# Performance work log

Hardware: AMD Instinct MI355X
Metric: run time of the kernel (lower is better)

Reference implementation:

```python
import jax, jax.numpy as jnp
import numpy as np

H = 64          # heightmap size (sqrt of in_channels=4096)
FEATS = [8, 16, 32, 64]
NEG_SLOPE = 0.01
EPS = 1e-12


def setup_inputs() -> dict:
    key = jax.random.key(0)
    ks = jax.random.split(key, 32)
    inp = {"x": jax.random.normal(ks[0], (16384, H * H), dtype=jnp.float32)}
    in_feat = H
    ki = 1
    for li, out_feat in enumerate(FEATS):
        bound = np.sqrt(6.0 / (in_feat + out_feat))  # xavier_uniform
        inp[f"w{li}"] = jax.random.uniform(ks[ki], (out_feat, in_feat), minval=-bound, maxval=bound, dtype=jnp.float32); ki += 1
        inp[f"b{li}"] = jnp.zeros((out_feat,), dtype=jnp.float32)
        inp[f"s{li}"] = jnp.ones((1,), dtype=jnp.float32)  # sigma parameter
        in_feat = out_feat
    compress_in = H * FEATS[-1]
    inp["wm0"] = jax.random.normal(ks[ki], (80, compress_in), dtype=jnp.float32) * 0.02; ki += 1
    inp["bm0"] = jnp.zeros((80,), dtype=jnp.float32)
    inp["wm1"] = jax.random.normal(ks[ki], (60, 80), dtype=jnp.float32) * 0.02; ki += 1
    inp["bm1"] = jnp.zeros((60,), dtype=jnp.float32)
    return inp


def _gauss_layer(x, dist_sq, sigma, w, b):
    # x: [B, H, Cin] ; dist_sq: [H, H] ; w: [Cout, Cin]
    xp = jnp.einsum('bhc,oc->bho', x, w) + b
    k = jnp.exp(-dist_sq / (2.0 * sigma[0] ** 2))                 # [H, H]
    k = k / jnp.maximum(jnp.sum(k, axis=-1, keepdims=True), EPS)  # L1 normalize
    out = jnp.einsum('ij,bjc->bic', k, xp)
    return jax.nn.leaky_relu(out, NEG_SLOPE)


def reference(x, w0, b0, s0, w1, b1, s1, w2, b2, s2, w3, b3, s3, wm0, bm0, wm1, bm1):
    B = x.shape[0]
    h = x.reshape(B, H, H)
    idx = jnp.arange(H, dtype=x.dtype)
    dist_sq = (idx[:, None] - idx[None, :]) ** 2  # coords are 1-D row indices
    for sigma, w, b in ((s0, w0, b0), (s1, w1, b1), (s2, w2, b2), (s3, w3, b3)):
        h = _gauss_layer(h, dist_sq, sigma, w, b)
    h = h.reshape(B, -1)                              # [B, H*64]
    h = jax.nn.leaky_relu(h @ wm0.T + bm0, NEG_SLOPE)
    h = jax.nn.leaky_relu(h @ wm1.T + bm1, NEG_SLOPE)
    return h
```

## Files before the change

kernel.cpp:

```cpp
#include <hip/hip_runtime.h>


typedef _Float16 f16x8 __attribute__((ext_vector_type(8)));
typedef _Float16 f16x4 __attribute__((ext_vector_type(4)));
typedef __fp16   hf2   __attribute__((ext_vector_type(2)));
typedef float    f32x4 __attribute__((ext_vector_type(4)));

#define KT_OFF    327680
#define W0P_OFF   344064
#define W1P_OFF   345088
#define W2P_OFF   345344
#define W3P_OFF   345856

__global__ void prep_all(const float* __restrict__ s0, const float* __restrict__ s1,
                         const float* __restrict__ s2, const float* __restrict__ s3,
                         const float* __restrict__ w0, const float* __restrict__ w1,
                         const float* __restrict__ w2, const float* __restrict__ w3,
                         const float* __restrict__ wm0, _Float16* __restrict__ base) {
  int bid = blockIdx.x, tid = threadIdx.x;
  if (bid < 1280) {
    int idx = bid * 256 + tid;
    int kc = idx / 2560, rem = idx % 2560;
    int n = rem >> 5, o = rem & 31;
    base[idx] = (_Float16)wm0[n * 4096 + kc * 32 + o];
  } else if (bid == 1280) {
    int li = tid >> 6, i = tid & 63;
    float sg = (li == 0) ? s0[0] : (li == 1) ? s1[0] : (li == 2) ? s2[0] : s3[0];
    float denom = 2.0f * sg * sg;
    float sum = 0.0f;
    for (int j = 0; j < 64; ++j) {
      float d = (float)(i - j);
      sum += expf(-(d * d) / denom);
    }
    float inv = 1.0f / fmaxf(sum, 1e-12f);
    for (int j = 0; j < 64; ++j) {
      float d = (float)(i - j);
      base[KT_OFF + (li * 64 + i) * 64 + j] = (_Float16)(expf(-(d * d) / denom) * inv);
    }
  } else {
    for (int r = tid; r < 3840; r += 256) {
      float v;
      if (r < 1024)      { int o = r >> 6, c = r & 63;             v = (o < 8) ? w0[o * 64 + c] : 0.0f; }
      else if (r < 1280) { int q = r - 1024; int o = q >> 4, c = q & 15; v = (c < 8) ? w1[o * 8 + c] : 0.0f; }
      else if (r < 1792) { int q = r - 1280; int o = q >> 4, c = q & 15; v = w2[o * 16 + c]; }
      else               { int q = r - 1792; int o = q >> 5, c = q & 31; v = w3[o * 32 + c]; }
      base[W0P_OFF + r] = (_Float16)v;
    }
  }
}

__device__ __forceinline__ float leaky(float v) { return v > 0.0f ? v : 0.01f * v; }

__device__ __forceinline__ f16x4 pk4(float a, float b, float c, float d) {
  union { f16x4 v; hf2 p[2]; } u;
  u.p[0] = __builtin_amdgcn_cvt_pkrtz(a, b);
  u.p[1] = __builtin_amdgcn_cvt_pkrtz(c, d);
  return u.v;
}

__device__ __forceinline__ int swz(int sx, int row, int c) {
  return row * 64 + ((((c >> 3) ^ (row & 7) ^ sx) & 7) << 3) + (c & 7);
}

#define DS_FENCE() __builtin_amdgcn_sched_barrier(0x7F)

__device__ __forceinline__ f16x8 ldf(const _Float16* p) { return *(const f16x8*)p; }
__device__ __forceinline__ f16x4 ldf4(const _Float16* p) { return *(const f16x4*)p; }

template<int NT, int KC>
__device__ __forceinline__ void stage_a_pre(_Float16* P, int sx,
                                            const f16x8* wf, const float* bv,
                                            int lo, int hi) {
  DS_FENCE();
  f16x8 a[4][KC];
#pragma unroll
  for (int mt = 0; mt < 4; ++mt)
#pragma unroll
    for (int kc = 0; kc < KC; ++kc)
      a[mt][kc] = ldf(P + swz(sx, mt * 16 + lo, kc * 32 + hi * 8));
  DS_FENCE();
#pragma unroll
  for (int mt = 0; mt < 4; ++mt)
#pragma unroll
    for (int nt = 0; nt < NT; ++nt) {
      f32x4 acc = {bv[nt], bv[nt], bv[nt], bv[nt]};
#pragma unroll
      for (int kc = 0; kc < KC; ++kc)
        acc = __builtin_amdgcn_mfma_f32_16x16x32_f16(a[mt][kc], wf[nt * KC + kc], acc, 0, 0, 0);
      *(f16x4*)(P + swz(sx, nt * 16 + lo, mt * 16 + hi * 4)) =
          pk4(acc[0], acc[1], acc[2], acc[3]);
    }
}

template<int NT>
__device__ __forceinline__ void stage_a16_pre(_Float16* P, int sx,
                                              const f16x4* wf, const float* bv,
                                              int lo, int hi) {
  DS_FENCE();
  f16x4 a[4];
#pragma unroll
  for (int mt = 0; mt < 4; ++mt)
    a[mt] = ldf4(P + swz(sx, mt * 16 + lo, hi * 4));
  DS_FENCE();
#pragma unroll
  for (int mt = 0; mt < 4; ++mt)
#pragma unroll
    for (int nt = 0; nt < NT; ++nt) {
      f32x4 acc = {bv[nt], bv[nt], bv[nt], bv[nt]};
      acc = __builtin_amdgcn_mfma_f32_16x16x16f16(a[mt], wf[nt], acc, 0, 0, 0);
      *(f16x4*)(P + swz(sx, nt * 16 + lo, mt * 16 + hi * 4)) =
          pk4(acc[0], acc[1], acc[2], acc[3]);
    }
}

template<int MT>
__device__ __forceinline__ void stage_b_pre(_Float16* P, int sx,
                                            const f16x8* kb, int lo, int hi) {
  DS_FENCE();
  f16x8 ax[MT][2];
#pragma unroll
  for (int ot = 0; ot < MT; ++ot)
#pragma unroll
    for (int kc = 0; kc < 2; ++kc)
      ax[ot][kc] = ldf(P + swz(sx, ot * 16 + lo, kc * 32 + hi * 8));
  DS_FENCE();
#pragma unroll
  for (int ot = 0; ot < MT; ++ot)
#pragma unroll
    for (int nt = 0; nt < 4; ++nt) {
      f32x4 acc = {0.0f, 0.0f, 0.0f, 0.0f};
#pragma unroll
      for (int kc = 0; kc < 2; ++kc)
        acc = __builtin_amdgcn_mfma_f32_16x16x32_f16(ax[ot][kc], kb[nt * 2 + kc], acc, 0, 0, 0);
      *(f16x4*)(P + swz(sx, nt * 16 + lo, ot * 16 + hi * 4)) =
          pk4(leaky(acc[0]), leaky(acc[1]), leaky(acc[2]), leaky(acc[3]));
    }
}

__global__ __launch_bounds__(1024, 4)
void fused(const float* __restrict__ x,
           const float* __restrict__ bb0, const float* __restrict__ bb1,
           const float* __restrict__ bb2, const float* __restrict__ bb3,
           const _Float16* __restrict__ wsh,
           const float* __restrict__ bm0, const float* __restrict__ wm1,
           const float* __restrict__ bm1, float* __restrict__ out, int B) {
  __shared__ _Float16 lds[16][4096];
  const int tid = threadIdx.x;
  const int wv = tid >> 6, lane = tid & 63;
  const int lo = lane & 15, hi = lane >> 4;
  const int smp0 = blockIdx.x * 16;
  int smp = smp0 + wv;  if (smp >= B) smp = B - 1;
  _Float16* P = lds[wv];
  const int sx = wv;
  const _Float16* kt = wsh + KT_OFF;

  float bv0 = (lo < 8) ? bb0[lo] : 0.0f;
  float bv1 = bb1[lo];
  float bv2[2] = {bb2[lo], bb2[16 + lo]};
  float bv3[4] = {bb3[lo], bb3[16 + lo], bb3[32 + lo], bb3[48 + lo]};

  f16x8 wf0[2];
#pragma unroll
  for (int kc = 0; kc < 2; ++kc)
    wf0[kc] = ldf(wsh + W0P_OFF + lo * 64 + kc * 32 + hi * 8);
  f16x8 kbA[8];
#pragma unroll
  for (int nt = 0; nt < 4; ++nt)
#pragma unroll
    for (int kc = 0; kc < 2; ++kc)
      kbA[nt * 2 + kc] = ldf(kt + 0 * 4096 + (nt * 16 + lo) * 64 + kc * 32 + hi * 8);

  const float* xr = x + (size_t)smp * 4096;
  f16x8 a0[4][2];
#pragma unroll
  for (int mt = 0; mt < 4; ++mt)
#pragma unroll
    for (int kc = 0; kc < 2; ++kc) {
      const float4* p4 = (const float4*)(xr + (mt * 16 + lo) * 64 + kc * 32 + hi * 8);
      float4 v0 = p4[0], v1 = p4[1];
      union { f16x8 v; hf2 p[4]; } u;
      u.p[0] = __builtin_amdgcn_cvt_pkrtz(v0.x, v0.y);
      u.p[1] = __builtin_amdgcn_cvt_pkrtz(v0.z, v0.w);
      u.p[2] = __builtin_amdgcn_cvt_pkrtz(v1.x, v1.y);
      u.p[3] = __builtin_amdgcn_cvt_pkrtz(v1.z, v1.w);
      a0[mt][kc] = u.v;
    }
  DS_FENCE();
#pragma unroll
  for (int mt = 0; mt < 4; ++mt) {
    f32x4 acc = {bv0, bv0, bv0, bv0};
#pragma unroll
    for (int kc = 0; kc < 2; ++kc)
      acc = __builtin_amdgcn_mfma_f32_16x16x32_f16(a0[mt][kc], wf0[kc], acc, 0, 0, 0);
    *(f16x4*)(P + swz(sx, lo, mt * 16 + hi * 4)) =
        pk4(acc[0], acc[1], acc[2], acc[3]);
  }

  f16x4 wfA1[1];
  wfA1[0] = ldf4(wsh + W1P_OFF + lo * 16 + hi * 4);
  stage_b_pre<1>(P, sx, kbA, lo, hi);

  f16x8 kbB[8];
#pragma unroll
  for (int nt = 0; nt < 4; ++nt)
#pragma unroll
    for (int kc = 0; kc < 2; ++kc)
      kbB[nt * 2 + kc] = ldf(kt + 1 * 4096 + (nt * 16 + lo) * 64 + kc * 32 + hi * 8);
  stage_a16_pre<1>(P, sx, wfA1, &bv1, lo, hi);

  f16x4 wfA2[2];
#pragma unroll
  for (int nt = 0; nt < 2; ++nt)
    wfA2[nt] = ldf4(wsh + W2P_OFF + (nt * 16 + lo) * 16 + hi * 4);
  stage_b_pre<1>(P, sx, kbB, lo, hi);

  f16x8 kbC[8];
#pragma unroll
  for (int nt = 0; nt < 4; ++nt)
#pragma unroll
    for (int kc = 0; kc < 2; ++kc)
      kbC[nt * 2 + kc] = ldf(kt + 2 * 4096 + (nt * 16 + lo) * 64 + kc * 32 + hi * 8);
  stage_a16_pre<2>(P, sx, wfA2, bv2, lo, hi);

  f16x8 wfA3[4];
#pragma unroll
  for (int nt = 0; nt < 4; ++nt)
    wfA3[nt] = ldf(wsh + W3P_OFF + (nt * 16 + lo) * 32 + hi * 8);
  stage_b_pre<2>(P, sx, kbC, lo, hi);

  f16x8 kbD[8];
#pragma unroll
  for (int nt = 0; nt < 4; ++nt)
#pragma unroll
    for (int kc = 0; kc < 2; ++kc)
      kbD[nt * 2 + kc] = ldf(kt + 3 * 4096 + (nt * 16 + lo) * 64 + kc * 32 + hi * 8);
  stage_a_pre<4, 1>(P, sx, wfA3, bv3, lo, hi);

  stage_b_pre<4>(P, sx, kbD, lo, hi);

  __syncthreads();

  f32x4 acc[5];
#pragma unroll
  for (int nt = 0; nt < 5; ++nt) { f32x4 z = {0.0f, 0.0f, 0.0f, 0.0f}; acc[nt] = z; }

  const _Float16* ap = &lds[lo][0];
#pragma unroll 2
  for (int it = 0; it < 8; ++it) {
    int kc = wv * 8 + it;
    int row = kc >> 1, cc = (kc & 1) * 32 + hi * 8;
    f16x8 a = *(const f16x8*)(ap + swz(lo, row, cc));
    const _Float16* bp = wsh + (size_t)kc * 2560 + lo * 32 + hi * 8;
#pragma unroll
    for (int nt = 0; nt < 5; ++nt) {
      f16x8 b = *(const f16x8*)(bp + nt * 512);
      acc[nt] = __builtin_amdgcn_mfma_f32_16x16x32_f16(a, b, acc[nt], 0, 0, 0);
    }
  }
  __syncthreads();

  float* scr = (float*)&lds[0][0];
#pragma unroll
  for (int nt = 0; nt < 5; ++nt)
#pragma unroll
    for (int r = 0; r < 4; ++r)
      scr[wv * 1280 + (hi * 4 + r) * 80 + nt * 16 + lo] = acc[nt][r];
  __syncthreads();

  float* h1 = scr + 20480;
  for (int e = tid; e < 1280; e += 1024) {
    int m = e / 80, n = e - m * 80;
    float v = bm0[n];
#pragma unroll
    for (int w = 0; w < 16; ++w) v += scr[w * 1280 + e];
    h1[e] = leaky(v);
  }
  __syncthreads();

  for (int e = tid; e < 960; e += 1024) {
    int m = e / 60, n = e - m * 60;
    float v = bm1[n];
    const float4* hr = (const float4*)(h1 + m * 80);
    const float4* wr = (const float4*)(wm1 + n * 80);
#pragma unroll
    for (int k2 = 0; k2 < 20; ++k2) {
      float4 hv = hr[k2], wv4 = wr[k2];
      v += hv.x * wv4.x + hv.y * wv4.y + hv.z * wv4.z + hv.w * wv4.w;
    }
    int s = smp0 + m;
    if (s < B) out[(size_t)s * 60 + n] = leaky(v);
  }
}

extern "C" void kernel_launch(void* const* d_in, const int* in_sizes, int n_in,
                              void* d_out, int out_size, void* d_ws, size_t ws_size,
                              hipStream_t stream) {
  const float* x   = (const float*)d_in[0];
  const float* w0  = (const float*)d_in[1];
  const float* b0  = (const float*)d_in[2];
  const float* s0  = (const float*)d_in[3];
  const float* w1  = (const float*)d_in[4];
  const float* b1  = (const float*)d_in[5];
  const float* s1  = (const float*)d_in[6];
  const float* w2  = (const float*)d_in[7];
  const float* b2  = (const float*)d_in[8];
  const float* s2  = (const float*)d_in[9];
  const float* w3  = (const float*)d_in[10];
  const float* b3  = (const float*)d_in[11];
  const float* s3  = (const float*)d_in[12];
  const float* wm0 = (const float*)d_in[13];
  const float* bm0 = (const float*)d_in[14];
  const float* wm1 = (const float*)d_in[15];
  const float* bm1 = (const float*)d_in[16];
  float* out = (float*)d_out;
  _Float16* wsh = (_Float16*)d_ws;

  int B = in_sizes[0] / 4096;

  prep_all<<<1282, 256, 0, stream>>>(s0, s1, s2, s3, w0, w1, w2, w3, wm0, wsh);
  fused<<<(B + 15) / 16, 1024, 0, stream>>>(x, b0, b1, b2, b3, wsh, bm0, wm1, bm1, out, B);
}
```

Measured before the change: 176.0 us.

## Keep Gaussian layer chain in registers via MFMA output-as-input layouts

Replaces the per-stage LDS round-trips (write MFMA results to swizzled shared memory, fence, reload) with a register-resident chain. It uses 16x16x16 MFMAs whose f16x4 accumulator layout directly feeds the next MFMA's operand, alternating which side holds the activation. Only the final layer writes to LDS for the compression GEMM. This removes LDS traffic and scheduling fences, but doubles the MFMA instruction count by using the smaller K=16 variant and raises register pressure.

```diff
diff --git a/kernel.cpp b/kernel.cpp
--- a/kernel.cpp
+++ b/kernel.cpp
@@ -62,80 +62,11 @@
   return row * 64 + ((((c >> 3) ^ (row & 7) ^ sx) & 7) << 3) + (c & 7);
 }
 
-#define DS_FENCE() __builtin_amdgcn_sched_barrier(0x7F)
-
 __device__ __forceinline__ f16x8 ldf(const _Float16* p) { return *(const f16x8*)p; }
 __device__ __forceinline__ f16x4 ldf4(const _Float16* p) { return *(const f16x4*)p; }
 
-template<int NT, int KC>
-__device__ __forceinline__ void stage_a_pre(_Float16* P, int sx,
-                                            const f16x8* wf, const float* bv,
-                                            int lo, int hi) {
-  DS_FENCE();
-  f16x8 a[4][KC];
-#pragma unroll
-  for (int mt = 0; mt < 4; ++mt)
-#pragma unroll
-    for (int kc = 0; kc < KC; ++kc)
-      a[mt][kc] = ldf(P + swz(sx, mt * 16 + lo, kc * 32 + hi * 8));
-  DS_FENCE();
-#pragma unroll
-  for (int mt = 0; mt < 4; ++mt)
-#pragma unroll
-    for (int nt = 0; nt < NT; ++nt) {
-      f32x4 acc = {bv[nt], bv[nt], bv[nt], bv[nt]};
-#pragma unroll
-      for (int kc = 0; kc < KC; ++kc)
-        acc = __builtin_amdgcn_mfma_f32_16x16x32_f16(a[mt][kc], wf[nt * KC + kc], acc, 0, 0, 0);
-      *(f16x4*)(P + swz(sx, nt * 16 + lo, mt * 16 + hi * 4)) =
-          pk4(acc[0], acc[1], acc[2], acc[3]);
-    }
-}
-
-template<int NT>
-__device__ __forceinline__ void stage_a16_pre(_Float16* P, int sx,
-                                              const f16x4* wf, const float* bv,
-                                              int lo, int hi) {
-  DS_FENCE();
-  f16x4 a[4];
-#pragma unroll
-  for (int mt = 0; mt < 4; ++mt)
-    a[mt] = ldf4(P + swz(sx, mt * 16 + lo, hi * 4));
-  DS_FENCE();
-#pragma unroll
-  for (int mt = 0; mt < 4; ++mt)
-#pragma unroll
-    for (int nt = 0; nt < NT; ++nt) {
-      f32x4 acc = {bv[nt], bv[nt], bv[nt], bv[nt]};
-      acc = __builtin_amdgcn_mfma_f32_16x16x16f16(a[mt], wf[nt], acc, 0, 0, 0);
-      *(f16x4*)(P + swz(sx, nt * 16 + lo, mt * 16 + hi * 4)) =
-          pk4(acc[0], acc[1], acc[2], acc[3]);
-    }
-}
-
-template<int MT>
-__device__ __forceinline__ void stage_b_pre(_Float16* P, int sx,
-                                            const f16x8* kb, int lo, int hi) {
-  DS_FENCE();
-  f16x8 ax[MT][2];
-#pragma unroll
-  for (int ot = 0; ot < MT; ++ot)
-#pragma unroll
-    for (int kc = 0; kc < 2; ++kc)
-      ax[ot][kc] = ldf(P + swz(sx, ot * 16 + lo, kc * 32 + hi * 8));
-  DS_FENCE();
-#pragma unroll
-  for (int ot = 0; ot < MT; ++ot)
-#pragma unroll
-    for (int nt = 0; nt < 4; ++nt) {
-      f32x4 acc = {0.0f, 0.0f, 0.0f, 0.0f};
-#pragma unroll
-      for (int kc = 0; kc < 2; ++kc)
-        acc = __builtin_amdgcn_mfma_f32_16x16x32_f16(ax[ot][kc], kb[nt * 2 + kc], acc, 0, 0, 0);
-      *(f16x4*)(P + swz(sx, nt * 16 + lo, ot * 16 + hi * 4)) =
-          pk4(leaky(acc[0]), leaky(acc[1]), leaky(acc[2]), leaky(acc[3]));
-    }
-}
+#define MFMA16(A, B, C) __builtin_amdgcn_mfma_f32_16x16x16f16((A), (B), (C), 0, 0, 0)
+#define MFMA32(A, B, C) __builtin_amdgcn_mfma_f32_16x16x32_f16((A), (B), (C), 0, 0, 0)
 
 __global__ __launch_bounds__(1024, 4)
 void fused(const float* __restrict__ x,
@@ -159,21 +90,15 @@
   float bv2[2] = {bb2[lo], bb2[16 + lo]};
   float bv3[4] = {bb3[lo], bb3[16 + lo], bb3[32 + lo], bb3[48 + lo]};
 
+  const float* xr = x + (size_t)smp * 4096;
   f16x8 wf0[2];
 #pragma unroll
   for (int kc = 0; kc < 2; ++kc)
     wf0[kc] = ldf(wsh + W0P_OFF + lo * 64 + kc * 32 + hi * 8);
-  f16x8 kbA[8];
-#pragma unroll
-  for (int nt = 0; nt < 4; ++nt)
-#pragma unroll
-    for (int kc = 0; kc < 2; ++kc)
-      kbA[nt * 2 + kc] = ldf(kt + 0 * 4096 + (nt * 16 + lo) * 64 + kc * 32 + hi * 8);
-
-  const float* xr = x + (size_t)smp * 4096;
-  f16x8 a0[4][2];
-#pragma unroll
-  for (int mt = 0; mt < 4; ++mt)
+  f16x4 xp0[4];
+#pragma unroll
+  for (int mt = 0; mt < 4; ++mt) {
+    f32x4 acc = {bv0, bv0, bv0, bv0};
 #pragma unroll
     for (int kc = 0; kc < 2; ++kc) {
       const float4* p4 = (const float4*)(xr + (mt * 16 + lo) * 64 + kc * 32 + hi * 8);
@@ -183,60 +108,116 @@
       u.p[1] = __builtin_amdgcn_cvt_pkrtz(v0.z, v0.w);
       u.p[2] = __builtin_amdgcn_cvt_pkrtz(v1.x, v1.y);
       u.p[3] = __builtin_amdgcn_cvt_pkrtz(v1.z, v1.w);
-      a0[mt][kc] = u.v;
-    }
-  DS_FENCE();
+      acc = MFMA32(u.v, wf0[kc], acc);
+    }
+    xp0[mt] = pk4(acc[0], acc[1], acc[2], acc[3]);
+  }
+
+  f16x4 kb[4][4];
+#pragma unroll
+  for (int nt = 0; nt < 4; ++nt)
+#pragma unroll
+    for (int kc = 0; kc < 4; ++kc)
+      kb[nt][kc] = ldf4(kt + 0 * 4096 + (nt * 16 + lo) * 64 + kc * 16 + hi * 4);
+  f16x4 a1[4];
+#pragma unroll
+  for (int nt = 0; nt < 4; ++nt) {
+    f32x4 acc = {0.0f, 0.0f, 0.0f, 0.0f};
+#pragma unroll
+    for (int kc = 0; kc < 4; ++kc)
+      acc = MFMA16(xp0[kc], kb[nt][kc], acc);
+    a1[nt] = pk4(leaky(acc[0]), leaky(acc[1]), leaky(acc[2]), leaky(acc[3]));
+  }
+
+  f16x4 wf1 = ldf4(wsh + W1P_OFF + lo * 16 + hi * 4);
+  f16x4 xp1[4];
 #pragma unroll
   for (int mt = 0; mt < 4; ++mt) {
-    f32x4 acc = {bv0, bv0, bv0, bv0};
+    f32x4 acc = {bv1, bv1, bv1, bv1};
+    acc = MFMA16(a1[mt], wf1, acc);
+    xp1[mt] = pk4(acc[0], acc[1], acc[2], acc[3]);
+  }
+
+#pragma unroll
+  for (int nt = 0; nt < 4; ++nt)
+#pragma unroll
+    for (int kc = 0; kc < 4; ++kc)
+      kb[nt][kc] = ldf4(kt + 1 * 4096 + (nt * 16 + lo) * 64 + kc * 16 + hi * 4);
+  f16x4 a2[4];
+#pragma unroll
+  for (int nt = 0; nt < 4; ++nt) {
+    f32x4 acc = {0.0f, 0.0f, 0.0f, 0.0f};
+#pragma unroll
+    for (int kc = 0; kc < 4; ++kc)
+      acc = MFMA16(xp1[kc], kb[nt][kc], acc);
+    a2[nt] = pk4(leaky(acc[0]), leaky(acc[1]), leaky(acc[2]), leaky(acc[3]));
+  }
+
+  f16x4 wf2[2];
+#pragma unroll
+  for (int nt = 0; nt < 2; ++nt)
+    wf2[nt] = ldf4(wsh + W2P_OFF + (nt * 16 + lo) * 16 + hi * 4);
+  f16x4 xp2[4][2];
+#pragma unroll
+  for (int mt = 0; mt < 4; ++mt)
+#pragma unroll
+    for (int nt = 0; nt < 2; ++nt) {
+      f32x4 acc = {bv2[nt], bv2[nt], bv2[nt], bv2[nt]};
+      acc = MFMA16(a2[mt], wf2[nt], acc);
+      xp2[mt][nt] = pk4(acc[0], acc[1], acc[2], acc[3]);
+    }
+
+#pragma unroll
+  for (int nt = 0; nt < 4; ++nt)
+#pragma unroll
+    for (int kc = 0; kc < 4; ++kc)
+      kb[nt][kc] = ldf4(kt + 2 * 4096 + (nt * 16 + lo) * 64 + kc * 16 + hi * 4);
+  f16x4 a3[4][2];
+#pragma unroll
+  for (int ct = 0; ct < 4; ++ct)
+#pragma unroll
+    for (int rt = 0; rt < 2; ++rt) {
+      f32x4 acc = {0.0f, 0.0f, 0.0f, 0.0f};
+#pragma unroll
+      for (int kc = 0; kc < 4; ++kc)
+        acc = MFMA16(xp2[kc][rt], kb[ct][kc], acc);
+      a3[ct][rt] = pk4(leaky(acc[0]), leaky(acc[1]), leaky(acc[2]), leaky(acc[3]));
+    }
+
+  f16x4 wf3[4][2];
+#pragma unroll
+  for (int nt = 0; nt < 4; ++nt)
 #pragma unroll
     for (int kc = 0; kc < 2; ++kc)
-      acc = __builtin_amdgcn_mfma_f32_16x16x32_f16(a0[mt][kc], wf0[kc], acc, 0, 0, 0);
-    *(f16x4*)(P + swz(sx, lo, mt * 16 + hi * 4)) =
-        pk4(acc[0], acc[1], acc[2], acc[3]);
-  }
-
-  f16x4 wfA1[1];
-  wfA1[0] = ldf4(wsh + W1P_OFF + lo * 16 + hi * 4);
-  stage_b_pre<1>(P, sx, kbA, lo, hi);
-
-  f16x8 kbB[8];
-#pragma unroll
-  for (int nt = 0; nt < 4; ++nt)
-#pragma unroll
-    for (int kc = 0; kc < 2; ++kc)
-      kbB[nt * 2 + kc] = ldf(kt + 1 * 4096 + (nt * 16 + lo) * 64 + kc * 32 + hi * 8);
-  stage_a16_pre<1>(P, sx, wfA1, &bv1, lo, hi);
-
-  f16x4 wfA2[2];
-#pragma unroll
-  for (int nt = 0; nt < 2; ++nt)
-    wfA2[nt] = ldf4(wsh + W2P_OFF + (nt * 16 + lo) * 16 + hi * 4);
-  stage_b_pre<1>(P, sx, kbB, lo, hi);
-
-  f16x8 kbC[8];
-#pragma unroll
-  for (int nt = 0; nt < 4; ++nt)
-#pragma unroll
-    for (int kc = 0; kc < 2; ++kc)
-      kbC[nt * 2 + kc] = ldf(kt + 2 * 4096 + (nt * 16 + lo) * 64 + kc * 32 + hi * 8);
-  stage_a16_pre<2>(P, sx, wfA2, bv2, lo, hi);
-
-  f16x8 wfA3[4];
-#pragma unroll
-  for (int nt = 0; nt < 4; ++nt)
-    wfA3[nt] = ldf(wsh + W3P_OFF + (nt * 16 + lo) * 32 + hi * 8);
-  stage_b_pre<2>(P, sx, kbC, lo, hi);
-
-  f16x8 kbD[8];
-#pragma unroll
-  for (int nt = 0; nt < 4; ++nt)
-#pragma unroll
-    for (int kc = 0; kc < 2; ++kc)
-      kbD[nt * 2 + kc] = ldf(kt + 3 * 4096 + (nt * 16 + lo) * 64 + kc * 32 + hi * 8);
-  stage_a_pre<4, 1>(P, sx, wfA3, bv3, lo, hi);
-
-  stage_b_pre<4>(P, sx, kbD, lo, hi);
+      wf3[nt][kc] = ldf4(wsh + W3P_OFF + (nt * 16 + lo) * 32 + kc * 16 + hi * 4);
+  f16x4 xp3[4][4];
+#pragma unroll
+  for (int mt = 0; mt < 4; ++mt)
+#pragma unroll
+    for (int nt = 0; nt < 4; ++nt) {
+      f32x4 acc = {bv3[nt], bv3[nt], bv3[nt], bv3[nt]};
+#pragma unroll
+      for (int kc = 0; kc < 2; ++kc)
+        acc = MFMA16(a3[mt][kc], wf3[nt][kc], acc);
+      xp3[mt][nt] = pk4(acc[0], acc[1], acc[2], acc[3]);
+    }
+
+#pragma unroll
+  for (int nt = 0; nt < 4; ++nt)
+#pragma unroll
+    for (int kc = 0; kc < 4; ++kc)
+      kb[nt][kc] = ldf4(kt + 3 * 4096 + (nt * 16 + lo) * 64 + kc * 16 + hi * 4);
+#pragma unroll
+  for (int ct = 0; ct < 4; ++ct)
+#pragma unroll
+    for (int rt = 0; rt < 4; ++rt) {
+      f32x4 acc = {0.0f, 0.0f, 0.0f, 0.0f};
+#pragma unroll
+      for (int kc = 0; kc < 4; ++kc)
+        acc = MFMA16(xp3[kc][rt], kb[ct][kc], acc);
+      *(f16x4*)(P + swz(sx, ct * 16 + lo, rt * 16 + hi * 4)) =
+          pk4(leaky(acc[0]), leaky(acc[1]), leaky(acc[2]), leaky(acc[3]));
+    }
 
   __syncthreads();
 
@@ -254,7 +235,7 @@
 #pragma unroll
     for (int nt = 0; nt < 5; ++nt) {
       f16x8 b = *(const f16x8*)(bp + nt * 512);
-      acc[nt] = __builtin_amdgcn_mfma_f32_16x16x32_f16(a, b, acc[nt], 0, 0, 0);
+      acc[nt] = MFMA32(a, b, acc[nt]);
     }
   }
   __syncthreads();
```

After: 232.1 us. 31.8% more time.
